# Performance work log

Measured on AMD Instinct MI355X. Metric: run time of the kernel, lower is better.

The kernel has to match this reference:

```python
import jax, jax.numpy as jnp
import numpy as np
from jax import lax

EPS = 1e-5

def _per_sample_conv(x, w, stride):
    # x: [B,C,H,W], w: [B,O,I,3,3] -> one conv per sample (hypernetwork weights)
    def one(xi, wi):
        return lax.conv_general_dilated(
            xi[None], wi, window_strides=(stride, stride),
            padding=((1, 1), (1, 1)),
            dimension_numbers=('NCHW', 'OIHW', 'NCHW'))[0]
    return jax.vmap(one)(x, w)

def _batchnorm_train(x, gamma, beta):
    # torch BatchNorm2d training mode: batch stats over (N,H,W), biased var
    mean = jnp.mean(x, axis=(0, 2, 3), keepdims=True)
    var = jnp.var(x, axis=(0, 2, 3), keepdims=True)
    xn = (x - mean) * lax.rsqrt(var + EPS)
    return xn * gamma[None, :, None, None] + beta[None, :, None, None]

def setup_inputs() -> dict:
    key = jax.random.key(0)
    k1, k2, k3 = jax.random.split(key, 3)
    B, C, H, W = 32, 64, 112, 112
    x = jax.random.normal(k1, (B, C, H, W), dtype=jnp.float32)
    conv1_w = jax.random.normal(k2, (B, C, C, 3, 3), dtype=jnp.float32)
    conv2_w = jax.random.normal(k3, (B, C, C, 3, 3), dtype=jnp.float32)
    gamma1 = jnp.ones((C,), jnp.float32)
    beta1 = jnp.zeros((C,), jnp.float32)
    gamma2 = jnp.ones((C,), jnp.float32)
    beta2 = jnp.zeros((C,), jnp.float32)
    return {"x": x, "conv1_w": conv1_w, "conv2_w": conv2_w,
            "gamma1": gamma1, "beta1": beta1, "gamma2": gamma2, "beta2": beta2}

def reference(x, conv1_w, conv2_w, gamma1, beta1, gamma2, beta2):
    residual = x  # downsample=False -> IdentityLayer
    out = _per_sample_conv(x, conv1_w, stride=1)
    out = jax.nn.relu(_batchnorm_train(out, gamma1, beta1))
    out = _per_sample_conv(out, conv2_w, stride=1)
    out = _batchnorm_train(out, gamma2, beta2)
    return jax.nn.relu(out + residual)
```

## Files before the change

kernel.cpp:

```cpp
#include <hip/hip_runtime.h>

#define HW   112
#define HW2  12544
#define CH   64
#define NB   32
#define PRW  113
#define NP   12655
#define POFF 128
#define PS   13056
#define NPC  (NB*HW2)
#define TPX  784

using u16 = unsigned short;
typedef __attribute__((ext_vector_type(8))) short bf16x8;
typedef __attribute__((ext_vector_type(4))) float f32x4;

__device__ __forceinline__ float b2f(u16 u) {
    union { unsigned int i; float f; } c;
    c.i = ((unsigned int)u) << 16;
    return c.f;
}
__device__ __forceinline__ u16 f2b(float f) {
    union { float f; unsigned int i; } c;
    c.f = f;
    unsigned int x = c.i;
    x += 0x7fffu + ((x >> 16) & 1u);
    return (u16)(x >> 16);
}

__device__ __forceinline__ void gl2lds(const u16* g, u16* l) {
    __builtin_amdgcn_global_load_lds(
        (const __attribute__((address_space(1))) unsigned int*)g,
        (__attribute__((address_space(3))) unsigned int*)l, 16, 0, 0);
}

template<int MODE>
__global__ __launch_bounds__(448, 2)
void conv_mfma(const u16* __restrict__ img, const u16* __restrict__ wt,
               u16* __restrict__ outp, float* __restrict__ sums,
               const float* __restrict__ psums, const float* __restrict__ gamma,
               const float* __restrict__ beta)
{
    __shared__ u16 wl[36864];
    __shared__ u16 bt[32768];
    const int bid = (int)blockIdx.x;
    const int sid = (bid & 7) * 64 + (bid >> 3);
    const int b = sid >> 4, tile = sid & 15;
    const int p0 = tile * TPX;
    const int w0 = tile * 791 - 114;
    const int tid = threadIdx.x;
    const int lane = tid & 63, wave = tid >> 6;
    const int px = lane & 15, kg = lane >> 4;
    const u16* wtb = wt + (size_t)b * 36864;

    if (tid < 384) {
#pragma unroll
        for (int i = 0; i < 12; ++i) {
            const int c = i * 384 + tid;
            gl2lds(wtb + (size_t)c * 8, wl + (size_t)(c - lane) * 8);
        }
    }

    float sc0[8], bi0[8], sc1[8], bi1[8];
    if (MODE == 1) {
        const int q = tid & 3;
#pragma unroll
        for (int e = 0; e < 8; ++e) {
            int c0 = q * 8 + e, c1 = 32 + q * 8 + e;
            float m0 = psums[c0] * (1.f / NPC), m1 = psums[c1] * (1.f / NPC);
            float v0 = psums[64 + c0] * (1.f / NPC) - m0 * m0;
            float v1 = psums[64 + c1] * (1.f / NPC) - m1 * m1;
            sc0[e] = gamma[c0] * rsqrtf(v0 + 1e-5f); bi0[e] = beta[c0] - m0 * sc0[e];
            sc1[e] = gamma[c1] * rsqrtf(v1 + 1e-5f); bi1[e] = beta[c1] - m1 * sc1[e];
        }
    }

    {
        const u16* bp = img + ((size_t)(b * 2 + 0) * PS + POFF + w0) * 32;
        if (MODE == 0) {
#pragma unroll
            for (int i = 0; i < 9; ++i) {
                const int c = i * 448 + tid;
                gl2lds(bp + (size_t)c * 8, bt + (size_t)(c - lane) * 8);
            }
            if (wave == 6)
                gl2lds(bp + (size_t)(4032 + lane) * 8, bt + (size_t)4032 * 8);
        } else {
            for (int c = tid; c < 4096; c += 448) {
                bf16x8 v = *(const bf16x8*)(bp + c * 8);
                int pt = w0 + (c >> 2);
                bool val = ((unsigned)pt < (unsigned)NP) && (pt % PRW != PRW - 1);
#pragma unroll
                for (int e = 0; e < 8; ++e) {
                    float t = b2f((u16)v[e]) * sc0[e] + bi0[e];
                    t = (val && t > 0.f) ? t : 0.f;
                    v[e] = (short)f2b(t);
                }
                *(bf16x8*)(bt + c * 8) = v;
            }
        }
    }
    __syncthreads();

    int lsf[7];
#pragma unroll
    for (int f = 0; f < 7; ++f) {
        const int pix = p0 + (wave * 7 + f) * 16 + px;
        lsf[f] = pix + pix / HW - w0;
    }

    f32x4 acc[7][4];
#pragma unroll
    for (int f = 0; f < 7; ++f)
#pragma unroll
        for (int m = 0; m < 4; ++m) acc[f][m] = (f32x4)0.f;

#pragma unroll
    for (int h = 0; h < 2; ++h) {
        if (h == 1) {
            __syncthreads();
            const u16* bp = img + ((size_t)(b * 2 + 1) * PS + POFF + w0) * 32;
            if (MODE == 0) {
#pragma unroll
                for (int i = 0; i < 9; ++i) {
                    const int c = i * 448 + tid;
                    gl2lds(bp + (size_t)c * 8, bt + (size_t)(c - lane) * 8);
                }
                if (wave == 6)
                    gl2lds(bp + (size_t)(4032 + lane) * 8, bt + (size_t)4032 * 8);
            } else {
                for (int c = tid; c < 4096; c += 448) {
                    bf16x8 v = *(const bf16x8*)(bp + c * 8);
                    int pt = w0 + (c >> 2);
                    bool val = ((unsigned)pt < (unsigned)NP) && (pt % PRW != PRW - 1);
#pragma unroll
                    for (int e = 0; e < 8; ++e) {
                        float t = b2f((u16)v[e]) * sc1[e] + bi1[e];
                        t = (val && t > 0.f) ? t : 0.f;
                        v[e] = (short)f2b(t);
                    }
                    *(bf16x8*)(bt + c * 8) = v;
                }
            }
            __syncthreads();
        }
#pragma unroll
        for (int tap = 0; tap < 9; ++tap) {
            const int off = (tap / 3 - 1) * PRW + (tap % 3 - 1);
            bf16x8 Af[4];
#pragma unroll
            for (int m = 0; m < 4; ++m)
                Af[m] = *(const bf16x8*)(wl + h * 18432 + tap * 2048 + kg * 512 + (m * 16 + px) * 8);
#pragma unroll
            for (int f = 0; f < 7; ++f) {
                bf16x8 Bf = *(const bf16x8*)(bt + (lsf[f] + off) * 32 + kg * 8);
#pragma unroll
                for (int m = 0; m < 4; ++m)
                    acc[f][m] = __builtin_amdgcn_mfma_f32_16x16x32_bf16(Af[m], Bf, acc[f][m], 0, 0, 0);
            }
        }
    }

    float s_[4][4], sq[4][4];
#pragma unroll
    for (int m = 0; m < 4; ++m)
#pragma unroll
        for (int q = 0; q < 4; ++q) { s_[m][q] = 0.f; sq[m][q] = 0.f; }

#pragma unroll
    for (int f = 0; f < 7; ++f) {
        const int pix  = p0 + (wave * 7 + f) * 16 + px;
        const int slot = pix + pix / HW;
#pragma unroll
        for (int m = 0; m < 4; ++m) {
            float v0 = acc[f][m][0], v1 = acc[f][m][1], v2 = acc[f][m][2], v3 = acc[f][m][3];
            s_[m][0] += v0; s_[m][1] += v1; s_[m][2] += v2; s_[m][3] += v3;
            sq[m][0] += v0 * v0; sq[m][1] += v1 * v1;
            sq[m][2] += v2 * v2; sq[m][3] += v3 * v3;
            uint2 pk;
            pk.x = ((unsigned)f2b(v1) << 16) | f2b(v0);
            pk.y = ((unsigned)f2b(v3) << 16) | f2b(v2);
            if (MODE == 0) {
                u16* dst = outp + ((size_t)(b * 2 + (m >> 1)) * PS + POFF + slot) * 32
                                + (m & 1) * 16 + kg * 4;
                *(uint2*)dst = pk;
            } else {
                u16* dst = outp + ((size_t)b * HW2 + pix) * 64 + m * 16 + kg * 4;
                *(uint2*)dst = pk;
            }
        }
    }
#pragma unroll
    for (int off = 1; off < 16; off <<= 1) {
#pragma unroll
        for (int m = 0; m < 4; ++m)
#pragma unroll
            for (int q = 0; q < 4; ++q) {
                s_[m][q] += __shfl_xor(s_[m][q], off);
                sq[m][q] += __shfl_xor(sq[m][q], off);
            }
    }
    __syncthreads();
    float* red = (float*)bt;
    if (px == 0) {
#pragma unroll
        for (int m = 0; m < 4; ++m)
#pragma unroll
            for (int q = 0; q < 4; ++q) {
                int c = m * 16 + kg * 4 + q;
                red[wave * 128 + c]      = s_[m][q];
                red[wave * 128 + 64 + c] = sq[m][q];
            }
    }
    __syncthreads();
    if (tid < 128) {
        float t = 0.f;
#pragma unroll
        for (int k = 0; k < 7; ++k) t += red[k * 128 + tid];
        atomicAdd(&sums[tid], t);
    }
}

__global__ __launch_bounds__(256)
void xpad_kernel(const float* __restrict__ x, u16* __restrict__ img)
{
    const int b  = blockIdx.y;
    const int y  = blockIdx.x * 2 + (threadIdx.x >> 7);
    const int px = threadIdx.x & 127;
    if (px >= HW) return;
    const float* xr = x + (size_t)b * CH * HW2 + (size_t)y * HW + px;
#pragma unroll
    for (int cg = 0; cg < 8; ++cg) {
        bf16x8 pk;
#pragma unroll
        for (int j = 0; j < 8; ++j)
            pk[j] = (short)f2b(xr[(size_t)(cg * 8 + j) * HW2]);
        u16* op = img + ((size_t)(b * 2 + (cg >> 2)) * PS + POFF + (size_t)y * PRW + px) * 32
                      + (cg & 3) * 8;
        *(bf16x8*)op = pk;
    }
}

__global__ void border_kernel(u16* __restrict__ a, u16* __restrict__ y1,
                              float* __restrict__ st)
{
    if (blockIdx.x == 256) {
        if (threadIdx.x < 256) st[threadIdx.x] = 0.f;
        return;
    }
    int t = blockIdx.x * 256 + threadIdx.x;
    u16* buf = (t >= 32768) ? y1 : a;
    int t2 = t & 32767;
    int bh = t2 >> 9;
    int s  = t2 & 511;
    int slot;
    if (s < POFF)            slot = s;
    else if (s < POFF + 273) slot = POFF + NP + (s - POFF);
    else                     slot = POFF + (s - (POFF + 273)) * PRW + (PRW - 1);
    float4* q = (float4*)(buf + ((size_t)bh * PS + slot) * 32);
#pragma unroll
    for (int i = 0; i < 4; ++i) q[i] = (float4){0.f, 0.f, 0.f, 0.f};
}

__global__ __launch_bounds__(256)
void repack2_kernel(const float* __restrict__ w1, const float* __restrict__ w2,
                    u16* __restrict__ wt1, u16* __restrict__ wt2)
{
    int i = blockIdx.x * 256 + threadIdx.x;
    const int N = NB * 36864;
    const float* w = (i < N) ? w1 : w2;
    u16* wt = (i < N) ? wt1 : wt2;
    int o = (i < N) ? i : i - N;
    int b = o / 36864, r = o - b * 36864;
    int half = r / 18432; r -= half * 18432;
    int tap  = r / 2048;  r -= tap * 2048;
    int kq   = r / 512;   r -= kq * 512;
    int co   = r / 8;
    int ci   = half * 32 + kq * 8 + (r & 7);
    wt[o] = f2b(w[(((size_t)b * 64 + co) * 64 + ci) * 9 + tap]);
}

__global__ __launch_bounds__(256)
void finalize_kernel(const u16* __restrict__ y2, const float* __restrict__ sums,
                     const float* __restrict__ gamma, const float* __restrict__ beta,
                     const float* __restrict__ x, float* __restrict__ out)
{
    __shared__ float lt[64][116];
    __shared__ float sbl[128];
    const int b = blockIdx.y, y = blockIdx.x;
    const int tid = threadIdx.x;
    if (tid < 64) {
        float mean = sums[tid] * (1.f / NPC);
        float var  = sums[64 + tid] * (1.f / NPC) - mean * mean;
        float sc   = gamma[tid] * rsqrtf(var + 1e-5f);
        sbl[tid]      = sc;
        sbl[64 + tid] = beta[tid] - mean * sc;
    }
    __syncthreads();
    const u16* rowp = y2 + ((size_t)b * HW2 + (size_t)y * HW) * 64;
    {
        const int cg = tid & 7;
        float sc[8], bi[8];
#pragma unroll
        for (int e = 0; e < 8; ++e) { sc[e] = sbl[cg * 8 + e]; bi[e] = sbl[64 + cg * 8 + e]; }
        for (int t = tid; t < HW * 8; t += 256) {
            int px = t >> 3;
            bf16x8 v = *(const bf16x8*)(rowp + px * 64 + cg * 8);
#pragma unroll
            for (int e = 0; e < 8; ++e)
                lt[cg * 8 + e][px] = b2f((u16)v[e]) * sc[e] + bi[e];
        }
    }
    __syncthreads();
    {
        const int c = tid >> 2, xg = (tid & 3) * 28;
        size_t base = ((size_t)b * CH + c) * HW2 + (size_t)y * HW + xg;
#pragma unroll
        for (int i = 0; i < 7; ++i) {
            float4 xv = *(const float4*)(x + base + i * 4);
            float4 r;
            r.x = fmaxf(lt[c][xg + i * 4 + 0] + xv.x, 0.f);
            r.y = fmaxf(lt[c][xg + i * 4 + 1] + xv.y, 0.f);
            r.z = fmaxf(lt[c][xg + i * 4 + 2] + xv.z, 0.f);
            r.w = fmaxf(lt[c][xg + i * 4 + 3] + xv.w, 0.f);
            *(float4*)(out + base + i * 4) = r;
        }
    }
}

extern "C" void kernel_launch(void* const* d_in, const int* in_sizes, int n_in,
                              void* d_out, int out_size, void* d_ws, size_t ws_size,
                              hipStream_t stream)
{
    const float* x  = (const float*)d_in[0];
    const float* w1 = (const float*)d_in[1];
    const float* w2 = (const float*)d_in[2];
    const float* g1 = (const float*)d_in[3];
    const float* b1 = (const float*)d_in[4];
    const float* g2 = (const float*)d_in[5];
    const float* b2 = (const float*)d_in[6];
    float* out = (float*)d_out;

    char* ws = (char*)d_ws;
    u16*   imgA = (u16*)ws;
    u16*   y2c  = (u16*)ws;
    float* st   = (float*)(ws + (size_t)(56u << 20));
    float* sums1 = st, *sums2 = st + 128;
    char*  oc   = (char*)d_out;
    u16*   y1p  = (u16*)oc;
    u16*   wt1  = (u16*)(oc + (size_t)(54u << 20));
    u16*   wt2  = (u16*)(oc + (size_t)(58u << 20));

    border_kernel<<<257, 256, 0, stream>>>(imgA, y1p, st);
    xpad_kernel<<<dim3(56, 32), 256, 0, stream>>>(x, imgA);
    repack2_kernel<<<9216, 256, 0, stream>>>(w1, w2, wt1, wt2);

    conv_mfma<0><<<512, 448, 0, stream>>>(imgA, wt1, y1p, sums1, st, g1, b1);
    conv_mfma<1><<<512, 448, 0, stream>>>(y1p, wt2, y2c, sums2, sums1, g1, b1);
    finalize_kernel<<<dim3(112, 32), 256, 0, stream>>>(y2c, sums2, g2, b2, x, out);
}
```

Before: 208.3 us.

## Fuse input padding/bf16 conversion into first conv and drop border kernel

Removes the separate xpad and border-zeroing kernels. The first convolution now reads fp32 x directly, converts it to bf16 while staging into LDS, and writes zeros for padding positions in-kernel. Zeroing of the stats buffer moves into an extra block of the weight repack kernel. This saves two launches and a full intermediate write/read of the padded bf16 image. In exchange, conv1 loses its asynchronous global-to-LDS loads and does strided per-channel fp32 loads, which may expose more load latency.

After: 191.9 us. 1.09x faster.

```diff
diff --git a/kernel.cpp b/kernel.cpp
--- a/kernel.cpp
+++ b/kernel.cpp
@@ -36,7 +36,8 @@
 
 template<int MODE>
 __global__ __launch_bounds__(448, 2)
-void conv_mfma(const u16* __restrict__ img, const u16* __restrict__ wt,
+void conv_mfma(const float* __restrict__ xf, const u16* __restrict__ img,
+               const u16* __restrict__ wt,
                u16* __restrict__ outp, float* __restrict__ sums,
                const float* __restrict__ psums, const float* __restrict__ gamma,
                const float* __restrict__ beta)
@@ -74,30 +75,35 @@
             sc1[e] = gamma[c1] * rsqrtf(v1 + 1e-5f); bi1[e] = beta[c1] - m1 * sc1[e];
         }
     }
+    const float* xb = (MODE == 0) ? xf + (size_t)b * CH * HW2 : nullptr;
 
     {
         const u16* bp = img + ((size_t)(b * 2 + 0) * PS + POFF + w0) * 32;
-        if (MODE == 0) {
-#pragma unroll
-            for (int i = 0; i < 9; ++i) {
-                const int c = i * 448 + tid;
-                gl2lds(bp + (size_t)c * 8, bt + (size_t)(c - lane) * 8);
-            }
-            if (wave == 6)
-                gl2lds(bp + (size_t)(4032 + lane) * 8, bt + (size_t)4032 * 8);
-        } else {
-            for (int c = tid; c < 4096; c += 448) {
-                bf16x8 v = *(const bf16x8*)(bp + c * 8);
-                int pt = w0 + (c >> 2);
+        for (int c = tid; c < 4096; c += 448) {
+            const int pt = w0 + (c >> 2);
+            bf16x8 v = (bf16x8)0;
+            if (MODE == 0) {
+                if ((unsigned)pt < (unsigned)NP) {
+                    int y  = (unsigned)pt / PRW;
+                    int xc = pt - y * PRW;
+                    if (xc != PRW - 1) {
+                        const float* src = xb + (size_t)((c & 3) * 8) * HW2 + y * HW + xc;
+#pragma unroll
+                        for (int e = 0; e < 8; ++e)
+                            v[e] = (short)f2b(src[(size_t)e * HW2]);
+                    }
+                }
+            } else {
                 bool val = ((unsigned)pt < (unsigned)NP) && (pt % PRW != PRW - 1);
+                bf16x8 r = *(const bf16x8*)(bp + c * 8);
 #pragma unroll
                 for (int e = 0; e < 8; ++e) {
-                    float t = b2f((u16)v[e]) * sc0[e] + bi0[e];
+                    float t = b2f((u16)r[e]) * sc0[e] + bi0[e];
                     t = (val && t > 0.f) ? t : 0.f;
                     v[e] = (short)f2b(t);
                 }
-                *(bf16x8*)(bt + c * 8) = v;
-            }
+            }
+            *(bf16x8*)(bt + c * 8) = v;
         }
     }
     __syncthreads();
@@ -120,27 +126,31 @@
         if (h == 1) {
             __syncthreads();
             const u16* bp = img + ((size_t)(b * 2 + 1) * PS + POFF + w0) * 32;
-            if (MODE == 0) {
-#pragma unroll
-                for (int i = 0; i < 9; ++i) {
-                    const int c = i * 448 + tid;
-                    gl2lds(bp + (size_t)c * 8, bt + (size_t)(c - lane) * 8);
-                }
-                if (wave == 6)
-                    gl2lds(bp + (size_t)(4032 + lane) * 8, bt + (size_t)4032 * 8);
-            } else {
-                for (int c = tid; c < 4096; c += 448) {
-                    bf16x8 v = *(const bf16x8*)(bp + c * 8);
-                    int pt = w0 + (c >> 2);
+            for (int c = tid; c < 4096; c += 448) {
+                const int pt = w0 + (c >> 2);
+                bf16x8 v = (bf16x8)0;
+                if (MODE == 0) {
+                    if ((unsigned)pt < (unsigned)NP) {
+                        int y  = (unsigned)pt / PRW;
+                        int xc = pt - y * PRW;
+                        if (xc != PRW - 1) {
+                            const float* src = xb + (size_t)(32 + (c & 3) * 8) * HW2 + y * HW + xc;
+#pragma unroll
+                            for (int e = 0; e < 8; ++e)
+                                v[e] = (short)f2b(src[(size_t)e * HW2]);
+                        }
+                    }
+                } else {
                     bool val = ((unsigned)pt < (unsigned)NP) && (pt % PRW != PRW - 1);
+                    bf16x8 r = *(const bf16x8*)(bp + c * 8);
 #pragma unroll
                     for (int e = 0; e < 8; ++e) {
-                        float t = b2f((u16)v[e]) * sc1[e] + bi1[e];
+                        float t = b2f((u16)r[e]) * sc1[e] + bi1[e];
                         t = (val && t > 0.f) ? t : 0.f;
                         v[e] = (short)f2b(t);
                     }
-                    *(bf16x8*)(bt + c * 8) = v;
                 }
+                *(bf16x8*)(bt + c * 8) = v;
             }
             __syncthreads();
         }
@@ -222,50 +232,14 @@
 }
 
 __global__ __launch_bounds__(256)
-void xpad_kernel(const float* __restrict__ x, u16* __restrict__ img)
+void repack2_kernel(const float* __restrict__ w1, const float* __restrict__ w2,
+                    u16* __restrict__ wt1, u16* __restrict__ wt2,
+                    float* __restrict__ st)
 {
-    const int b  = blockIdx.y;
-    const int y  = blockIdx.x * 2 + (threadIdx.x >> 7);
-    const int px = threadIdx.x & 127;
-    if (px >= HW) return;
-    const float* xr = x + (size_t)b * CH * HW2 + (size_t)y * HW + px;
-#pragma unroll
-    for (int cg = 0; cg < 8; ++cg) {
-        bf16x8 pk;
-#pragma unroll
-        for (int j = 0; j < 8; ++j)
-            pk[j] = (short)f2b(xr[(size_t)(cg * 8 + j) * HW2]);
-        u16* op = img + ((size_t)(b * 2 + (cg >> 2)) * PS + POFF + (size_t)y * PRW + px) * 32
-                      + (cg & 3) * 8;
-        *(bf16x8*)op = pk;
-    }
-}
-
-__global__ void border_kernel(u16* __restrict__ a, u16* __restrict__ y1,
-                              float* __restrict__ st)
-{
-    if (blockIdx.x == 256) {
-        if (threadIdx.x < 256) st[threadIdx.x] = 0.f;
+    if (blockIdx.x == 9216) {
+        st[threadIdx.x] = 0.f;
         return;
     }
-    int t = blockIdx.x * 256 + threadIdx.x;
-    u16* buf = (t >= 32768) ? y1 : a;
-    int t2 = t & 32767;
-    int bh = t2 >> 9;
-    int s  = t2 & 511;
-    int slot;
-    if (s < POFF)            slot = s;
-    else if (s < POFF + 273) slot = POFF + NP + (s - POFF);
-    else                     slot = POFF + (s - (POFF + 273)) * PRW + (PRW - 1);
-    float4* q = (float4*)(buf + ((size_t)bh * PS + slot) * 32);
-#pragma unroll
-    for (int i = 0; i < 4; ++i) q[i] = (float4){0.f, 0.f, 0.f, 0.f};
-}
-
-__global__ __launch_bounds__(256)
-void repack2_kernel(const float* __restrict__ w1, const float* __restrict__ w2,
-                    u16* __restrict__ wt1, u16* __restrict__ wt2)
-{
     int i = blockIdx.x * 256 + threadIdx.x;
     const int N = NB * 36864;
     const float* w = (i < N) ? w1 : w2;
@@ -342,7 +316,6 @@
     float* out = (float*)d_out;
 
     char* ws = (char*)d_ws;
-    u16*   imgA = (u16*)ws;
     u16*   y2c  = (u16*)ws;
     float* st   = (float*)(ws + (size_t)(56u << 20));
     float* sums1 = st, *sums2 = st + 128;
@@ -351,11 +324,9 @@
     u16*   wt1  = (u16*)(oc + (size_t)(54u << 20));
     u16*   wt2  = (u16*)(oc + (size_t)(58u << 20));
 
-    border_kernel<<<257, 256, 0, stream>>>(imgA, y1p, st);
-    xpad_kernel<<<dim3(56, 32), 256, 0, stream>>>(x, imgA);
-    repack2_kernel<<<9216, 256, 0, stream>>>(w1, w2, wt1, wt2);
-
-    conv_mfma<0><<<512, 448, 0, stream>>>(imgA, wt1, y1p, sums1, st, g1, b1);
-    conv_mfma<1><<<512, 448, 0, stream>>>(y1p, wt2, y2c, sums2, sums1, g1, b1);
+    repack2_kernel<<<9217, 256, 0, stream>>>(w1, w2, wt1, wt2, st);
+
+    conv_mfma<0><<<512, 448, 0, stream>>>(x, nullptr, wt1, y1p, sums1, st, g1, b1);
+    conv_mfma<1><<<512, 448, 0, stream>>>(nullptr, y1p, wt2, y2c, sums2, sums1, g1, b1);
     finalize_kernel<<<dim3(112, 32), 256, 0, stream>>>(y2c, sums2, g2, b2, x, out);
 }
```
